# Optimization experiments

Hardware: AMD Instinct MI355X
Metric: run time of the kernel (lower is better)

The kernel has to match this reference:

```python
import jax, jax.numpy as jnp
import numpy as np

B, BINS, EMBED, HID, IND = 1, 500, 1024, 512, 128
POOL, MC_CROP, HIC_CROP = 5, 50, 10


def setup_inputs() -> dict:
    key = jax.random.key(0)
    ks = jax.random.split(key, 10)
    def w(k, shape, fan_in):
        return (jax.random.normal(k, shape, jnp.float32) / np.sqrt(fan_in)).astype(jnp.float32)
    return dict(
        x=jax.random.normal(ks[0], (B, BINS, EMBED), jnp.float32),
        # project MLP
        p_w1=w(ks[1], (EMBED, HID), EMBED), p_b1=jnp.zeros((HID,), jnp.float32),
        p_w2=w(ks[2], (HID, HID), HID), p_b2=jnp.zeros((HID,), jnp.float32),
        # pairattn_cop stub: per-pair linears (micro at full res, hic after 5x5 avg-pool)
        micro_w=w(ks[3], (HID, IND), HID), micro_b=jnp.zeros((IND,), jnp.float32),
        hic_w=w(ks[4], (HID, IND), HID), hic_b=jnp.zeros((IND,), jnp.float32),
        # prediction heads
        head_mc_w=w(ks[5], (IND, 2), IND), head_mc_b=jnp.zeros((2,), jnp.float32),
        head_ih_w1=w(ks[6], (IND, IND // 2), IND), head_ih_b1=jnp.zeros((IND // 2,), jnp.float32),
        head_ih_w2=w(ks[7], (IND // 2, 2), IND // 2), head_ih_b2=jnp.zeros((2,), jnp.float32),
        head_hic_w=w(ks[8], (IND, 3), IND), head_hic_b=jnp.zeros((3,), jnp.float32),
    )


def reference(x, p_w1, p_b1, p_w2, p_b2, micro_w, micro_b, hic_w, hic_b,
              head_mc_w, head_mc_b, head_ih_w1, head_ih_b1, head_ih_w2, head_ih_b2,
              head_hic_w, head_hic_b):
    # project: Linear -> ReLU -> Linear
    h = jax.nn.relu(x @ p_w1 + p_b1) @ p_w2 + p_b2            # [B, bins, HID]
    # output_head: fused pairwise outer-sum mean + scaled elementwise dot
    xi = h[:, :, None, :]                                      # [B, bins, 1, HID]
    xj = h[:, None, :, :]                                      # [B, 1, bins, HID]
    pair = (xi + xj) * 0.5 + xi * xj * (1.0 / np.sqrt(HID))    # [B, bins, bins, HID]
    # pairattn_cop stub
    micro = pair @ micro_w + micro_b                           # [B, bins, bins, IND]
    nb = BINS // POOL
    hic_in = pair.reshape(B, nb, POOL, nb, POOL, HID).mean(axis=(2, 4))  # [B, nb, nb, HID]
    hic = hic_in @ hic_w + hic_b                               # [B, nb, nb, IND]
    # prediction heads with crops
    mc = micro[:, MC_CROP:-MC_CROP, MC_CROP:-MC_CROP, :]       # [B, 400, 400, IND]
    out_mc = mc @ head_mc_w + head_mc_b
    out_ih = jax.nn.relu(mc @ head_ih_w1 + head_ih_b1) @ head_ih_w2 + head_ih_b2
    hc = hic[:, HIC_CROP:-HIC_CROP, HIC_CROP:-HIC_CROP, :]     # [B, 80, 80, IND]
    out_hic = hc @ head_hic_w + head_hic_b
    return (out_mc, out_ih, micro, out_hic)
```

## Files before the change

### kernel.cpp

```cpp
#include <hip/hip_runtime.h>

#define BINS 500
#define HID  512
#define INDD 128
#define PAIR_S 0.044194173824159216f

#define OFF_MC    0
#define OFF_IH    320000
#define OFF_MICRO 640000
#define OFF_HIC   32640000

#define WS_U     0
#define WS_MWT   64000
#define WS_HBF   96768
#define WS_H     256000
#define WS_HBAR  512000
#define WS_HWT   563200
#define WS_W1CT  595968

typedef __bf16 bf16;
typedef bf16 bf16x4 __attribute__((ext_vector_type(4)));
typedef bf16 bf16x8 __attribute__((ext_vector_type(8)));
typedef float f32x4 __attribute__((ext_vector_type(4)));

__device__ __forceinline__ bf16x8 join8(bf16x4 lo, bf16x4 hi) {
  return __builtin_shufflevector(lo, hi, 0, 1, 2, 3, 4, 5, 6, 7);
}
__device__ __forceinline__ bf16x4 cvt4(float a, float b, float c, float d) {
  bf16x4 r; r[0] = (bf16)a; r[1] = (bf16)b; r[2] = (bf16)c; r[3] = (bf16)d; return r;
}

__global__ void zero_init(float* __restrict__ ws) {
  int idx = (blockIdx.x * 256 + threadIdx.x) * 4;
  float4 z = {0.f, 0.f, 0.f, 0.f};
  *(float4*)(ws + idx) = z;
  *(float4*)(ws + WS_H + idx) = z;
}

__global__ __launch_bounds__(256, 2)
void gemm_ks(const float* __restrict__ A, const float* __restrict__ B,
             const float* __restrict__ abias, float* __restrict__ C,
             int M, int N, int K_per, int a_relu, float scale) {
  __shared__ float a_lds[64][36];
  __shared__ float bt_lds[64][36];
  const int t = threadIdx.x;
  const int w = t >> 6, l = t & 63;
  const int lr = l & 15, g = l >> 4;
  const int r0 = blockIdx.x * 64, n0 = blockIdx.y * 64;
  const int kbase = blockIdx.z * K_per;
  f32x4 acc[4] = {};
  for (int kq = 0; kq < K_per; kq += 32) {
    const int k0 = kbase + kq;
    {
      int row = t >> 2, kc = (t & 3) * 8;
      int gr = r0 + row; gr = gr < M ? gr : M - 1;
      const float* src = A + (size_t)gr * K_per * gridDim.z + k0 + kc;
      float4 v0 = *(const float4*)src;
      float4 v1 = *(const float4*)(src + 4);
      if (abias) {
        const float* bp = abias + k0 + kc;
        v0.x += bp[0]; v0.y += bp[1]; v0.z += bp[2]; v0.w += bp[3];
        v1.x += bp[4]; v1.y += bp[5]; v1.z += bp[6]; v1.w += bp[7];
        if (a_relu) {
          v0.x = fmaxf(v0.x, 0.f); v0.y = fmaxf(v0.y, 0.f);
          v0.z = fmaxf(v0.z, 0.f); v0.w = fmaxf(v0.w, 0.f);
          v1.x = fmaxf(v1.x, 0.f); v1.y = fmaxf(v1.y, 0.f);
          v1.z = fmaxf(v1.z, 0.f); v1.w = fmaxf(v1.w, 0.f);
        }
      }
      *(float4*)&a_lds[row][kc]     = v0;
      *(float4*)&a_lds[row][kc + 4] = v1;
    }
    {
      int n = t & 63, ks = (t >> 6) * 8;
      const float* src = B + (size_t)(k0 + ks) * N + n0 + n;
      #pragma unroll
      for (int s = 0; s < 8; s++) bt_lds[n][ks + s] = src[(size_t)s * N];
    }
    __syncthreads();
    bf16x8 ahi, alo;
    {
      int row = w * 16 + lr;
      float4 u0 = *(const float4*)&a_lds[row][g * 8];
      float4 u1 = *(const float4*)&a_lds[row][g * 8 + 4];
      float v[8] = {u0.x, u0.y, u0.z, u0.w, u1.x, u1.y, u1.z, u1.w};
      #pragma unroll
      for (int e = 0; e < 8; e++) {
        bf16 h = (bf16)v[e];
        ahi[e] = h; alo[e] = (bf16)(v[e] - (float)h);
      }
    }
    #pragma unroll
    for (int fn = 0; fn < 4; fn++) {
      int col = fn * 16 + lr;
      float4 u0 = *(const float4*)&bt_lds[col][g * 8];
      float4 u1 = *(const float4*)&bt_lds[col][g * 8 + 4];
      float v[8] = {u0.x, u0.y, u0.z, u0.w, u1.x, u1.y, u1.z, u1.w};
      bf16x8 bhi, blo;
      #pragma unroll
      for (int e = 0; e < 8; e++) {
        bf16 h = (bf16)v[e];
        bhi[e] = h; blo[e] = (bf16)(v[e] - (float)h);
      }
      acc[fn] = __builtin_amdgcn_mfma_f32_16x16x32_bf16(ahi, bhi, acc[fn], 0, 0, 0);
      acc[fn] = __builtin_amdgcn_mfma_f32_16x16x32_bf16(ahi, blo, acc[fn], 0, 0, 0);
      acc[fn] = __builtin_amdgcn_mfma_f32_16x16x32_bf16(alo, bhi, acc[fn], 0, 0, 0);
    }
    __syncthreads();
  }
  #pragma unroll
  for (int fn = 0; fn < 4; fn++) {
    int col = n0 + fn * 16 + lr;
    #pragma unroll
    for (int r = 0; r < 4; r++) {
      int row = r0 + w * 16 + g * 4 + r;
      if (row < M) atomicAdd(&C[(size_t)row * N + col], acc[fn][r] * scale);
    }
  }
}

__global__ void post_h(const float* __restrict__ h, const float* __restrict__ b2,
                       const float* __restrict__ micro_w,
                       const float* __restrict__ hic_w, const float* __restrict__ w_ih1,
                       const float* __restrict__ w_mc, float* __restrict__ ws) {
  int g = blockIdx.x * 256 + threadIdx.x;
  if (g < 256000) {
    bf16* hbf = (bf16*)(ws + WS_HBF);
    int k = g & (HID - 1);
    hbf[g] = (bf16)(h[g] + b2[k]);
  } else if (g < 256000 + 65536) {
    int gg = g - 256000;
    int n = gg >> 9, k = gg & 511;
    bf16* mwt = (bf16*)(ws + WS_MWT);
    mwt[gg] = (bf16)(PAIR_S * micro_w[k * INDD + n]);
  } else if (g < 256000 + 65536 + 51200) {
    int gg = g - (256000 + 65536);
    int a = gg >> 9, k = gg & (HID - 1);
    const float* p = h + (size_t)(a * 5) * HID + k;
    ws[WS_HBAR + gg] = 0.2f * (p[0] + p[HID] + p[2 * HID] + p[3 * HID] + p[4 * HID]) + b2[k];
  } else if (g < 256000 + 65536 + 51200 + 65536) {
    int gg = g - (256000 + 65536 + 51200);
    int n = gg >> 9, k = gg & 511;
    bf16* hwt = (bf16*)(ws + WS_HWT);
    hwt[gg] = (bf16)hic_w[k * INDD + n];
  } else if (g < 256000 + 65536 + 51200 + 65536 + 10240) {
    int gg = g - (256000 + 65536 + 51200 + 65536);
    int n = gg >> 7, k = gg & 127;
    float v = 0.f;
    if (n < 64) v = w_ih1[k * 64 + n];
    else if (n < 66) v = w_mc[k * 2 + (n - 64)];
    bf16* w1c = (bf16*)(ws + WS_W1CT);
    w1c[gg] = (bf16)v;
  } else if (g < 256000 + 65536 + 51200 + 65536 + 10240 + 64000) {
    int gg = g - (256000 + 65536 + 51200 + 65536 + 10240);
    ws[WS_U + gg] = 0.f;
  }
}

__global__ __launch_bounds__(256, 4)
void fused_micro(const float* __restrict__ wsf, const float* __restrict__ micro_b,
                 float* __restrict__ out) {
  __shared__ bf16 Ht[2][128 * 32];
  __shared__ bf16 Bt[2][128 * 32];
  const int t = threadIdx.x;
  const int wv = t >> 6, l = t & 63;
  const int wj = wv >> 1, wn = wv & 1;
  const int lr = l & 15, g = l >> 4;
  const int i  = blockIdx.x;
  const int j0 = blockIdx.y * 128;
  const bf16* Hbf = (const bf16*)(wsf + WS_HBF);
  const bf16* mwt = (const bf16*)(wsf + WS_MWT);
  const float* U  = wsf + WS_U;
  const int bn = t >> 1, bh = t & 1;
  const int arow   = l >> 2;
  const int achunk = (l & 3) ^ ((l >> 3) & 3);
  const bf16* hbi = Hbf + (size_t)i * HID;
  f32x4 acc[4][4] = {};

  #pragma unroll
  for (int q = 0; q < 2; q++) {
    int row = wv * 32 + q * 16 + arow;
    int jj = j0 + row; jj = jj < BINS ? jj : BINS - 1;
    __builtin_amdgcn_global_load_lds(
        (const __attribute__((address_space(1))) void*)(Hbf + (size_t)jj * HID + achunk * 8),
        (__attribute__((address_space(3))) void*)(&Ht[0][(wv * 32 + q * 16) * 32]),
        16, 0, 0);
  }
  {
    bf16x8 w0 = *(const bf16x8*)(mwt + (size_t)bn * HID + bh * 16);
    bf16x8 w1 = *(const bf16x8*)(mwt + (size_t)bn * HID + bh * 16 + 8);
    bf16x8 h0 = *(const bf16x8*)(hbi + bh * 16);
    bf16x8 h1 = *(const bf16x8*)(hbi + bh * 16 + 8);
    bf16x8 o0, o1;
    #pragma unroll
    for (int e = 0; e < 8; e++) o0[e] = (bf16)((float)h0[e] * (float)w0[e]);
    #pragma unroll
    for (int e = 0; e < 8; e++) o1[e] = (bf16)((float)h1[e] * (float)w1[e]);
    const int sw = (bn >> 1) & 3;
    *(bf16x8*)(&Bt[0][0] + bn * 32 + ((bh * 2)     ^ sw) * 8) = o0;
    *(bf16x8*)(&Bt[0][0] + bn * 32 + ((bh * 2 + 1) ^ sw) * 8) = o1;
  }
  asm volatile("s_waitcnt vmcnt(0) lgkmcnt(0)" ::: "memory");
  __builtin_amdgcn_s_barrier();

  int cur = 0;
  for (int kt = 0; kt < 16; kt++) {
    const bf16* htc = &Ht[cur][0];
    const bf16* btc = &Bt[cur][0];
    bf16x8 w0, w1, h0, h1;
    if (kt < 15) {
      const int kn = (kt + 1) * 32;
      w0 = *(const bf16x8*)(mwt + (size_t)bn * HID + kn + bh * 16);
      w1 = *(const bf16x8*)(mwt + (size_t)bn * HID + kn + bh * 16 + 8);
      h0 = *(const bf16x8*)(hbi + kn + bh * 16);
      h1 = *(const bf16x8*)(hbi + kn + bh * 16 + 8);
      #pragma unroll
      for (int q = 0; q < 2; q++) {
        int row = wv * 32 + q * 16 + arow;
        int jj = j0 + row; jj = jj < BINS ? jj : BINS - 1;
        __builtin_amdgcn_global_load_lds(
            (const __attribute__((address_space(1))) void*)(Hbf + (size_t)jj * HID + kn + achunk * 8),
            (__attribute__((address_space(3))) void*)(&Ht[cur ^ 1][(wv * 32 + q * 16) * 32]),
            16, 0, 0);
      }
      asm volatile("s_waitcnt vmcnt(6)" ::: "memory");
    } else {
      asm volatile("s_waitcnt vmcnt(0)" ::: "memory");
    }
    bf16x8 af[4], bfr[4];
    const int s = g ^ ((lr >> 1) & 3);
    #pragma unroll
    for (int fm = 0; fm < 4; fm++)
      af[fm] = *(const bf16x8*)(htc + (wj * 64 + fm * 16 + lr) * 32 + s * 8);
    #pragma unroll
    for (int fn = 0; fn < 4; fn++)
      bfr[fn] = *(const bf16x8*)(btc + (wn * 64 + fn * 16 + lr) * 32 + s * 8);
    #pragma unroll
    for (int fm = 0; fm < 4; fm++)
      #pragma unroll
      for (int fn = 0; fn < 4; fn++)
        acc[fm][fn] = __builtin_amdgcn_mfma_f32_16x16x32_bf16(af[fm], bfr[fn], acc[fm][fn], 0, 0, 0);
    if (kt < 15) {
      bf16x8 o0, o1;
      #pragma unroll
      for (int e = 0; e < 8; e++) o0[e] = (bf16)((float)h0[e] * (float)w0[e]);
      #pragma unroll
      for (int e = 0; e < 8; e++) o1[e] = (bf16)((float)h1[e] * (float)w1[e]);
      bf16* btn = &Bt[cur ^ 1][0];
      const int sw = (bn >> 1) & 3;
      *(bf16x8*)(btn + bn * 32 + ((bh * 2)     ^ sw) * 8) = o0;
      *(bf16x8*)(btn + bn * 32 + ((bh * 2 + 1) ^ sw) * 8) = o1;
    }
    asm volatile("s_waitcnt lgkmcnt(0)" ::: "memory");
    __builtin_amdgcn_s_barrier();
    cur ^= 1;
  }

  float Ui[4];
  #pragma unroll
  for (int fn = 0; fn < 4; fn++) {
    int n = wn * 64 + fn * 16 + lr;
    Ui[fn] = U[(size_t)i * INDD + n] + micro_b[n];
  }
  #pragma unroll
  for (int fm = 0; fm < 4; fm++) {
    #pragma unroll
    for (int r = 0; r < 4; r++) {
      int j = j0 + wj * 64 + fm * 16 + g * 4 + r;
      if (j < BINS) {
        const float* Uj = U + (size_t)j * INDD;
        size_t base = (size_t)OFF_MICRO + ((size_t)i * BINS + j) * INDD;
        #pragma unroll
        for (int fn = 0; fn < 4; fn++) {
          int n = wn * 64 + fn * 16 + lr;
          out[base + n] = acc[fm][fn][r] + Ui[fn] + Uj[n];
        }
      }
    }
  }
}

__global__ __launch_bounds__(256, 2)
void heads_direct(const float* __restrict__ micro, const float* __restrict__ wsf,
                  const float* __restrict__ b1, const float* __restrict__ w2,
                  const float* __restrict__ bmc, const float* __restrict__ b2,
                  float* __restrict__ out) {
  const int t = threadIdx.x;
  const int wv = t >> 6, l = t & 63;
  const int lr = l & 15, g = l >> 4;
  const int mm0 = blockIdx.x * 256;
  const bf16* w1c = (const bf16*)(wsf + WS_W1CT);
  int mrow[4];
  #pragma unroll
  for (int fm = 0; fm < 4; fm++) {
    int mm = mm0 + wv * 64 + fm * 16 + lr;
    mrow[fm] = 25050 + mm + 100 * (mm / 400);
  }
  f32x4 acc[4][5] = {};
  #pragma unroll
  for (int kt = 0; kt < 4; kt++) {
    const int k0 = kt * 32;
    bf16x8 bfr[5];
    #pragma unroll
    for (int fn = 0; fn < 5; fn++) {
      int q = fn * 16 + lr;
      bfr[fn] = *(const bf16x8*)(w1c + q * 128 + k0 + g * 8);
    }
    #pragma unroll
    for (int fm = 0; fm < 4; fm++) {
      const float* src = micro + (size_t)mrow[fm] * INDD + k0 + g * 8;
      float4 v0 = *(const float4*)src;
      float4 v1 = *(const float4*)(src + 4);
      bf16x8 af = join8(cvt4(v0.x, v0.y, v0.z, v0.w), cvt4(v1.x, v1.y, v1.z, v1.w));
      #pragma unroll
      for (int fn = 0; fn < 5; fn++)
        acc[fm][fn] = __builtin_amdgcn_mfma_f32_16x16x32_bf16(af, bfr[fn], acc[fm][fn], 0, 0, 0);
    }
  }
  float w2a[4], w2b[4], b1v[4];
  #pragma unroll
  for (int fn = 0; fn < 4; fn++) {
    int q = fn * 16 + lr;
    w2a[fn] = w2[q * 2]; w2b[fn] = w2[q * 2 + 1]; b1v[fn] = b1[q];
  }
  float bm = (lr < 2) ? bmc[lr] : 0.f;
  float b2a = b2[0], b2bv = b2[1];
  #pragma unroll
  for (int fm = 0; fm < 4; fm++) {
    #pragma unroll
    for (int r = 0; r < 4; r++) {
      int m = wv * 64 + fm * 16 + g * 4 + r;
      float s0 = 0.f, s1 = 0.f;
      #pragma unroll
      for (int fn = 0; fn < 4; fn++) {
        float v = fmaxf(acc[fm][fn][r] + b1v[fn], 0.f);
        s0 += v * w2a[fn]; s1 += v * w2b[fn];
      }
      #pragma unroll
      for (int mk = 1; mk < 16; mk <<= 1) {
        s0 += __shfl_xor(s0, mk);
        s1 += __shfl_xor(s1, mk);
      }
      size_t mo = (size_t)(mm0 + m);
      if (lr == 0) {
        out[OFF_IH + mo * 2]     = s0 + b2a;
        out[OFF_IH + mo * 2 + 1] = s1 + b2bv;
      }
      if (lr < 2) out[OFF_MC + mo * 2 + lr] = acc[fm][4][r] + bm;
    }
  }
}

__device__ __forceinline__ bf16x4 pair4(float4 a, float4 b) {
  bf16x4 r;
  r[0] = (bf16)((a.x + b.x) * 0.5f + a.x * b.x * PAIR_S);
  r[1] = (bf16)((a.y + b.y) * 0.5f + a.y * b.y * PAIR_S);
  r[2] = (bf16)((a.z + b.z) * 0.5f + a.z * b.z * PAIR_S);
  r[3] = (bf16)((a.w + b.w) * 0.5f + a.w * b.w * PAIR_S);
  return r;
}

__global__ __launch_bounds__(256, 2)
void hic_kernel(const float* __restrict__ hbar, const float* __restrict__ wsf,
                const float* __restrict__ hicb, const float* __restrict__ whic,
                const float* __restrict__ bhic, float* __restrict__ out) {
  __shared__ float ha_lds[16][36];
  __shared__ float hb_lds[16][36];
  __shared__ bf16 pair_lds[256][36];
  __shared__ bf16 bt_lds[128][36];
  const int t = threadIdx.x;
  const int wv = t >> 6, l = t & 63;
  const int lr = l & 15, g = l >> 4;
  const int a0 = 10 + blockIdx.x * 16, b0 = 10 + blockIdx.y * 16;
  const bf16* hwt = (const bf16*)(wsf + WS_HWT);
  f32x4 acc[4][8] = {};
  for (int kt = 0; kt < 16; kt++) {
    const int k0 = kt * 32;
    if (t < 64) {
      int row = t >> 2, c = (t & 3) * 8;
      const float* src = hbar + (size_t)(a0 + row) * HID + k0 + c;
      *(float4*)&ha_lds[row][c]     = *(const float4*)src;
      *(float4*)&ha_lds[row][c + 4] = *(const float4*)(src + 4);
    } else if (t < 128) {
      int tt = t - 64;
      int row = tt >> 2, c = (tt & 3) * 8;
      const float* src = hbar + (size_t)(b0 + row) * HID + k0 + c;
      *(float4*)&hb_lds[row][c]     = *(const float4*)src;
      *(float4*)&hb_lds[row][c + 4] = *(const float4*)(src + 4);
    } else {
      int tt = t - 128;
      #pragma unroll
      for (int rep = 0; rep < 4; rep++) {
        int chunk = tt * 4 + rep;
        int n = chunk >> 2, part = chunk & 3;
        bf16x8 v = *(const bf16x8*)(hwt + (size_t)n * HID + k0 + part * 8);
        *(bf16x4*)&bt_lds[n][part * 8]     = __builtin_shufflevector(v, v, 0, 1, 2, 3);
        *(bf16x4*)&bt_lds[n][part * 8 + 4] = __builtin_shufflevector(v, v, 4, 5, 6, 7);
      }
    }
    __syncthreads();
    {
      int m = t;
      const float* pa = &ha_lds[m >> 4][0];
      const float* pb = &hb_lds[m & 15][0];
      #pragma unroll
      for (int c = 0; c < 4; c++) {
        float4 av0 = *(const float4*)(pa + c * 8);
        float4 av1 = *(const float4*)(pa + c * 8 + 4);
        float4 bv0 = *(const float4*)(pb + c * 8);
        float4 bv1 = *(const float4*)(pb + c * 8 + 4);
        *(bf16x4*)&pair_lds[m][c * 8]     = pair4(av0, bv0);
        *(bf16x4*)&pair_lds[m][c * 8 + 4] = pair4(av1, bv1);
      }
    }
    __syncthreads();
    bf16x8 af[4], bfr[8];
    #pragma unroll
    for (int fm = 0; fm < 4; fm++) {
      int row = wv * 64 + fm * 16 + lr;
      af[fm] = join8(*(const bf16x4*)&pair_lds[row][g * 8],
                     *(const bf16x4*)&pair_lds[row][g * 8 + 4]);
    }
    #pragma unroll
    for (int fn = 0; fn < 8; fn++) {
      int col = fn * 16 + lr;
      bfr[fn] = join8(*(const bf16x4*)&bt_lds[col][g * 8],
                      *(const bf16x4*)&bt_lds[col][g * 8 + 4]);
    }
    #pragma unroll
    for (int fm = 0; fm < 4; fm++)
      #pragma unroll
      for (int fn = 0; fn < 8; fn++)
        acc[fm][fn] = __builtin_amdgcn_mfma_f32_16x16x32_bf16(af[fm], bfr[fn], acc[fm][fn], 0, 0, 0);
    __syncthreads();
  }
  float wh0[8], wh1[8], wh2[8], hbv[8];
  #pragma unroll
  for (int fn = 0; fn < 8; fn++) {
    int n = fn * 16 + lr;
    wh0[fn] = whic[n * 3]; wh1[fn] = whic[n * 3 + 1]; wh2[fn] = whic[n * 3 + 2];
    hbv[fn] = hicb[n];
  }
  float bh0 = bhic[0], bh1 = bhic[1], bh2 = bhic[2];
  #pragma unroll
  for (int fm = 0; fm < 4; fm++) {
    #pragma unroll
    for (int r = 0; r < 4; r++) {
      int m = wv * 64 + fm * 16 + g * 4 + r;
      float s0 = 0.f, s1 = 0.f, s2 = 0.f;
      #pragma unroll
      for (int fn = 0; fn < 8; fn++) {
        float v = acc[fm][fn][r] + hbv[fn];
        s0 += v * wh0[fn]; s1 += v * wh1[fn]; s2 += v * wh2[fn];
      }
      #pragma unroll
      for (int mk = 1; mk < 16; mk <<= 1) {
        s0 += __shfl_xor(s0, mk);
        s1 += __shfl_xor(s1, mk);
        s2 += __shfl_xor(s2, mk);
      }
      if (lr == 0) {
        int aa = a0 + (m >> 4) - 10, bb = b0 + (m & 15) - 10;
        size_t o = (size_t)OFF_HIC + (size_t)(aa * 80 + bb) * 3;
        out[o] = s0 + bh0; out[o + 1] = s1 + bh1; out[o + 2] = s2 + bh2;
      }
    }
  }
}

extern "C" void kernel_launch(void* const* d_in, const int* in_sizes, int n_in,
                              void* d_out, int out_size, void* d_ws, size_t ws_size,
                              hipStream_t stream) {
  (void)in_sizes; (void)n_in; (void)out_size; (void)ws_size;
  const float* x    = (const float*)d_in[0];
  const float* pw1  = (const float*)d_in[1];
  const float* pb1  = (const float*)d_in[2];
  const float* pw2  = (const float*)d_in[3];
  const float* pb2  = (const float*)d_in[4];
  const float* mw   = (const float*)d_in[5];
  const float* mb   = (const float*)d_in[6];
  const float* hw   = (const float*)d_in[7];
  const float* hb   = (const float*)d_in[8];
  const float* wmc  = (const float*)d_in[9];
  const float* bmc  = (const float*)d_in[10];
  const float* wih1 = (const float*)d_in[11];
  const float* bih1 = (const float*)d_in[12];
  const float* wih2 = (const float*)d_in[13];
  const float* bih2 = (const float*)d_in[14];
  const float* whic = (const float*)d_in[15];
  const float* bhic = (const float*)d_in[16];
  float* out = (float*)d_out;
  float* ws  = (float*)d_ws;

  zero_init<<<250, 256, 0, stream>>>(ws);
  gemm_ks<<<dim3(8, 8, 4), 256, 0, stream>>>(x, pw1, nullptr, ws, 500, 512, 256, 0, 1.f);
  gemm_ks<<<dim3(8, 8, 2), 256, 0, stream>>>(ws, pw2, pb1, ws + WS_H, 500, 512, 256, 1, 1.f);
  post_h<<<2252, 256, 0, stream>>>(ws + WS_H, pb2, mw, hw, wih1, wmc, ws);
  gemm_ks<<<dim3(8, 2, 4), 256, 0, stream>>>(ws + WS_H, mw, pb2, ws + WS_U, 500, 128, 128, 0, 0.5f);
  fused_micro<<<dim3(500, 4), 256, 0, stream>>>(ws, mb, out);
  heads_direct<<<625, 256, 0, stream>>>(out + OFF_MICRO, ws, bih1, wih2, bmc, bih2, out);
  hic_kernel<<<dim3(5, 5), 256, 0, stream>>>(ws + WS_HBAR, ws, hb, whic, bhic, out);
}
```

Measured before the change: 167.3 us.

## Enlarge fused_micro tile to 256 rows, vectorize post_h, deepen split-K

fused_micro now runs 512-thread blocks that each cover 256 j-rows instead of 128. Each product of the i-row with micro_w is therefore built once per 256 rows, and each thread does a single 8-wide B-tile element instead of two. post_h is rewritten so each thread handles 8 elements with vectorized float4 and bf16x8 loads and stores, cutting its launch from 2252 blocks to 251. The projection GEMMs and the U GEMM split K further (more z-slices with smaller K chunks), which adds parallelism at the cost of more atomic adds. The larger tiles halve the fused_micro grid to 1000 blocks and double the LDS per block, which may lower occupancy and load balance.

```diff
diff --git a/kernel.cpp b/kernel.cpp
--- a/kernel.cpp
+++ b/kernel.cpp
@@ -124,54 +124,82 @@
                        const float* __restrict__ hic_w, const float* __restrict__ w_ih1,
                        const float* __restrict__ w_mc, float* __restrict__ ws) {
   int g = blockIdx.x * 256 + threadIdx.x;
-  if (g < 256000) {
-    bf16* hbf = (bf16*)(ws + WS_HBF);
-    int k = g & (HID - 1);
-    hbf[g] = (bf16)(h[g] + b2[k]);
-  } else if (g < 256000 + 65536) {
-    int gg = g - 256000;
+  if (g < 32000) {
+    int e = g * 8, k = e & (HID - 1);
+    float4 a0 = *(const float4*)(h + e),  a1 = *(const float4*)(h + e + 4);
+    float4 c0 = *(const float4*)(b2 + k), c1 = *(const float4*)(b2 + k + 4);
+    bf16x8 o;
+    o[0] = (bf16)(a0.x + c0.x); o[1] = (bf16)(a0.y + c0.y);
+    o[2] = (bf16)(a0.z + c0.z); o[3] = (bf16)(a0.w + c0.w);
+    o[4] = (bf16)(a1.x + c1.x); o[5] = (bf16)(a1.y + c1.y);
+    o[6] = (bf16)(a1.z + c1.z); o[7] = (bf16)(a1.w + c1.w);
+    *(bf16x8*)((bf16*)(ws + WS_HBF) + e) = o;
+  } else if (g < 40192) {
+    int gg = (g - 32000) * 8;
     int n = gg >> 9, k = gg & 511;
-    bf16* mwt = (bf16*)(ws + WS_MWT);
-    mwt[gg] = (bf16)(PAIR_S * micro_w[k * INDD + n]);
-  } else if (g < 256000 + 65536 + 51200) {
-    int gg = g - (256000 + 65536);
+    bf16x8 o;
+    #pragma unroll
+    for (int e = 0; e < 8; e++) o[e] = (bf16)(PAIR_S * micro_w[(size_t)(k + e) * INDD + n]);
+    *(bf16x8*)((bf16*)(ws + WS_MWT) + gg) = o;
+  } else if (g < 46592) {
+    int gg = (g - 40192) * 8;
     int a = gg >> 9, k = gg & (HID - 1);
     const float* p = h + (size_t)(a * 5) * HID + k;
-    ws[WS_HBAR + gg] = 0.2f * (p[0] + p[HID] + p[2 * HID] + p[3 * HID] + p[4 * HID]) + b2[k];
-  } else if (g < 256000 + 65536 + 51200 + 65536) {
-    int gg = g - (256000 + 65536 + 51200);
+    float s[8] = {};
+    #pragma unroll
+    for (int r = 0; r < 5; r++) {
+      float4 v0 = *(const float4*)(p + r * HID);
+      float4 v1 = *(const float4*)(p + r * HID + 4);
+      s[0] += v0.x; s[1] += v0.y; s[2] += v0.z; s[3] += v0.w;
+      s[4] += v1.x; s[5] += v1.y; s[6] += v1.z; s[7] += v1.w;
+    }
+    float4 c0 = *(const float4*)(b2 + k), c1 = *(const float4*)(b2 + k + 4);
+    float4 o0 = {s[0] * 0.2f + c0.x, s[1] * 0.2f + c0.y, s[2] * 0.2f + c0.z, s[3] * 0.2f + c0.w};
+    float4 o1 = {s[4] * 0.2f + c1.x, s[5] * 0.2f + c1.y, s[6] * 0.2f + c1.z, s[7] * 0.2f + c1.w};
+    *(float4*)(ws + WS_HBAR + gg)     = o0;
+    *(float4*)(ws + WS_HBAR + gg + 4) = o1;
+  } else if (g < 54784) {
+    int gg = (g - 46592) * 8;
     int n = gg >> 9, k = gg & 511;
-    bf16* hwt = (bf16*)(ws + WS_HWT);
-    hwt[gg] = (bf16)hic_w[k * INDD + n];
-  } else if (g < 256000 + 65536 + 51200 + 65536 + 10240) {
-    int gg = g - (256000 + 65536 + 51200 + 65536);
+    bf16x8 o;
+    #pragma unroll
+    for (int e = 0; e < 8; e++) o[e] = (bf16)hic_w[(size_t)(k + e) * INDD + n];
+    *(bf16x8*)((bf16*)(ws + WS_HWT) + gg) = o;
+  } else if (g < 56064) {
+    int gg = (g - 54784) * 8;
     int n = gg >> 7, k = gg & 127;
-    float v = 0.f;
-    if (n < 64) v = w_ih1[k * 64 + n];
-    else if (n < 66) v = w_mc[k * 2 + (n - 64)];
-    bf16* w1c = (bf16*)(ws + WS_W1CT);
-    w1c[gg] = (bf16)v;
-  } else if (g < 256000 + 65536 + 51200 + 65536 + 10240 + 64000) {
-    int gg = g - (256000 + 65536 + 51200 + 65536 + 10240);
-    ws[WS_U + gg] = 0.f;
-  }
-}
-
-__global__ __launch_bounds__(256, 4)
+    bf16x8 o;
+    #pragma unroll
+    for (int e = 0; e < 8; e++) {
+      float v = 0.f;
+      if (n < 64) v = w_ih1[(k + e) * 64 + n];
+      else if (n < 66) v = w_mc[(k + e) * 2 + (n - 64)];
+      o[e] = (bf16)v;
+    }
+    *(bf16x8*)((bf16*)(ws + WS_W1CT) + gg) = o;
+  } else if (g < 64064) {
+    int gg = (g - 56064) * 8;
+    float4 z = {0.f, 0.f, 0.f, 0.f};
+    *(float4*)(ws + WS_U + gg)     = z;
+    *(float4*)(ws + WS_U + gg + 4) = z;
+  }
+}
+
+__global__ __launch_bounds__(512, 4)
 void fused_micro(const float* __restrict__ wsf, const float* __restrict__ micro_b,
                  float* __restrict__ out) {
-  __shared__ bf16 Ht[2][128 * 32];
+  __shared__ bf16 Ht[2][256 * 32];
   __shared__ bf16 Bt[2][128 * 32];
   const int t = threadIdx.x;
   const int wv = t >> 6, l = t & 63;
   const int wj = wv >> 1, wn = wv & 1;
   const int lr = l & 15, g = l >> 4;
   const int i  = blockIdx.x;
-  const int j0 = blockIdx.y * 128;
+  const int j0 = blockIdx.y * 256;
   const bf16* Hbf = (const bf16*)(wsf + WS_HBF);
   const bf16* mwt = (const bf16*)(wsf + WS_MWT);
   const float* U  = wsf + WS_U;
-  const int bn = t >> 1, bh = t & 1;
+  const int bn = t >> 2, bq = t & 3;
   const int arow   = l >> 2;
   const int achunk = (l & 3) ^ ((l >> 3) & 3);
   const bf16* hbi = Hbf + (size_t)i * HID;
@@ -187,18 +215,13 @@
         16, 0, 0);
   }
   {
-    bf16x8 w0 = *(const bf16x8*)(mwt + (size_t)bn * HID + bh * 16);
-    bf16x8 w1 = *(const bf16x8*)(mwt + (size_t)bn * HID + bh * 16 + 8);
-    bf16x8 h0 = *(const bf16x8*)(hbi + bh * 16);
-    bf16x8 h1 = *(const bf16x8*)(hbi + bh * 16 + 8);
-    bf16x8 o0, o1;
-    #pragma unroll
-    for (int e = 0; e < 8; e++) o0[e] = (bf16)((float)h0[e] * (float)w0[e]);
-    #pragma unroll
-    for (int e = 0; e < 8; e++) o1[e] = (bf16)((float)h1[e] * (float)w1[e]);
-    const int sw = (bn >> 1) & 3;
-    *(bf16x8*)(&Bt[0][0] + bn * 32 + ((bh * 2)     ^ sw) * 8) = o0;
-    *(bf16x8*)(&Bt[0][0] + bn * 32 + ((bh * 2 + 1) ^ sw) * 8) = o1;
+    bf16x8 w = *(const bf16x8*)(mwt + (size_t)bn * HID + bq * 8);
+    bf16x8 hh = *(const bf16x8*)(hbi + bq * 8);
+    bf16x8 o;
+    #pragma unroll
+    for (int e = 0; e < 8; e++) o[e] = (bf16)((float)hh[e] * (float)w[e]);
+    const int slot = bq ^ ((bn >> 1) & 3);
+    *(bf16x8*)(&Bt[0][0] + bn * 32 + slot * 8) = o;
   }
   asm volatile("s_waitcnt vmcnt(0) lgkmcnt(0)" ::: "memory");
   __builtin_amdgcn_s_barrier();
@@ -207,13 +230,11 @@
   for (int kt = 0; kt < 16; kt++) {
     const bf16* htc = &Ht[cur][0];
     const bf16* btc = &Bt[cur][0];
-    bf16x8 w0, w1, h0, h1;
+    bf16x8 w, hh;
     if (kt < 15) {
       const int kn = (kt + 1) * 32;
-      w0 = *(const bf16x8*)(mwt + (size_t)bn * HID + kn + bh * 16);
-      w1 = *(const bf16x8*)(mwt + (size_t)bn * HID + kn + bh * 16 + 8);
-      h0 = *(const bf16x8*)(hbi + kn + bh * 16);
-      h1 = *(const bf16x8*)(hbi + kn + bh * 16 + 8);
+      w  = *(const bf16x8*)(mwt + (size_t)bn * HID + kn + bq * 8);
+      hh = *(const bf16x8*)(hbi + kn + bq * 8);
       #pragma unroll
       for (int q = 0; q < 2; q++) {
         int row = wv * 32 + q * 16 + arow;
@@ -223,7 +244,7 @@
             (__attribute__((address_space(3))) void*)(&Ht[cur ^ 1][(wv * 32 + q * 16) * 32]),
             16, 0, 0);
       }
-      asm volatile("s_waitcnt vmcnt(6)" ::: "memory");
+      asm volatile("s_waitcnt vmcnt(4)" ::: "memory");
     } else {
       asm volatile("s_waitcnt vmcnt(0)" ::: "memory");
     }
@@ -241,15 +262,11 @@
       for (int fn = 0; fn < 4; fn++)
         acc[fm][fn] = __builtin_amdgcn_mfma_f32_16x16x32_bf16(af[fm], bfr[fn], acc[fm][fn], 0, 0, 0);
     if (kt < 15) {
-      bf16x8 o0, o1;
-      #pragma unroll
-      for (int e = 0; e < 8; e++) o0[e] = (bf16)((float)h0[e] * (float)w0[e]);
-      #pragma unroll
-      for (int e = 0; e < 8; e++) o1[e] = (bf16)((float)h1[e] * (float)w1[e]);
-      bf16* btn = &Bt[cur ^ 1][0];
-      const int sw = (bn >> 1) & 3;
-      *(bf16x8*)(btn + bn * 32 + ((bh * 2)     ^ sw) * 8) = o0;
-      *(bf16x8*)(btn + bn * 32 + ((bh * 2 + 1) ^ sw) * 8) = o1;
+      bf16x8 o;
+      #pragma unroll
+      for (int e = 0; e < 8; e++) o[e] = (bf16)((float)hh[e] * (float)w[e]);
+      const int slot = bq ^ ((bn >> 1) & 3);
+      *(bf16x8*)(&Bt[cur ^ 1][0] + bn * 32 + slot * 8) = o;
     }
     asm volatile("s_waitcnt lgkmcnt(0)" ::: "memory");
     __builtin_amdgcn_s_barrier();
@@ -493,11 +510,11 @@
   float* ws  = (float*)d_ws;
 
   zero_init<<<250, 256, 0, stream>>>(ws);
-  gemm_ks<<<dim3(8, 8, 4), 256, 0, stream>>>(x, pw1, nullptr, ws, 500, 512, 256, 0, 1.f);
-  gemm_ks<<<dim3(8, 8, 2), 256, 0, stream>>>(ws, pw2, pb1, ws + WS_H, 500, 512, 256, 1, 1.f);
-  post_h<<<2252, 256, 0, stream>>>(ws + WS_H, pb2, mw, hw, wih1, wmc, ws);
-  gemm_ks<<<dim3(8, 2, 4), 256, 0, stream>>>(ws + WS_H, mw, pb2, ws + WS_U, 500, 128, 128, 0, 0.5f);
-  fused_micro<<<dim3(500, 4), 256, 0, stream>>>(ws, mb, out);
+  gemm_ks<<<dim3(8, 8, 8), 256, 0, stream>>>(x, pw1, nullptr, ws, 500, 512, 128, 0, 1.f);
+  gemm_ks<<<dim3(8, 8, 4), 256, 0, stream>>>(ws, pw2, pb1, ws + WS_H, 500, 512, 128, 1, 1.f);
+  post_h<<<251, 256, 0, stream>>>(ws + WS_H, pb2, mw, hw, wih1, wmc, ws);
+  gemm_ks<<<dim3(8, 2, 8), 256, 0, stream>>>(ws + WS_H, mw, pb2, ws + WS_U, 500, 128, 64, 0, 0.5f);
+  fused_micro<<<dim3(500, 2), 512, 0, stream>>>(ws, mb, out);
   heads_direct<<<625, 256, 0, stream>>>(out + OFF_MICRO, ws, bih1, wih2, bmc, bih2, out);
   hic_kernel<<<dim3(5, 5), 256, 0, stream>>>(ws + WS_HBAR, ws, hb, whic, bhic, out);
 }
```

New measurement: 149.3 us. -10.8%, faster.
